# Kernel tuning notes

Measured on AMD Instinct MI355X. Metric: run time of the kernel, lower is better.

Reference implementation:

```python
import jax, jax.numpy as jnp
import numpy as np

B, S, D, H, E, K, HID = 4, 1024, 1024, 16, 8, 2, 4096
HD = D // H


def _ln(x, g, b):
    m = x.mean(-1, keepdims=True)
    v = x.var(-1, keepdims=True)
    return (x - m) / jnp.sqrt(v + 1e-5) * g + b


def setup_inputs():
    key = jax.random.key(0)
    ks = jax.random.split(key, 12)
    p = lambda i, shape: jax.random.normal(ks[i], shape, jnp.float32) * 0.02
    return {
        "x": jax.random.normal(ks[0], (B, S, D), jnp.float32),
        "text_state": jax.random.normal(ks[1], (B, D), jnp.float32),
        "ln1_g": jnp.ones((D,), jnp.float32), "ln1_b": jnp.zeros((D,), jnp.float32),
        "wqkv": p(2, (D, 3 * D)), "bqkv": jnp.zeros((3 * D,), jnp.float32),
        "wo": p(3, (D, D)), "bo": jnp.zeros((D,), jnp.float32),
        "rel_bias": p(4, (H, 2 * S - 1)),
        "ln2_g": jnp.ones((D,), jnp.float32), "ln2_b": jnp.zeros((D,), jnp.float32),
        "cap_w": p(5, (D, D)), "cap_b": jnp.zeros((D,), jnp.float32),
        "gate_w": p(6, (D, E)), "gate_b": jnp.zeros((E,), jnp.float32),
        "w1": p(7, (E, D, HID)), "b1": jnp.zeros((E, HID), jnp.float32),
        "w2": p(8, (E, HID, D)), "b2": jnp.zeros((E, D), jnp.float32),
    }


def reference(x, text_state, ln1_g, ln1_b, wqkv, bqkv, wo, bo, rel_bias,
              ln2_g, ln2_b, cap_w, cap_b, gate_w, gate_b, w1, b1, w2, b2):
    # --- temporal-bias multi-head self-attention (pre-LN, residual) ---
    h = _ln(x, ln1_g, ln1_b)
    qkv = h @ wqkv + bqkv                          # [B,S,3D]
    q, k, v = jnp.split(qkv, 3, axis=-1)
    q = q.reshape(B, S, H, HD).transpose(0, 2, 1, 3)
    k = k.reshape(B, S, H, HD).transpose(0, 2, 1, 3)
    v = v.reshape(B, S, H, HD).transpose(0, 2, 1, 3)
    scores = jnp.einsum('bhqd,bhkd->bhqk', q, k) / jnp.sqrt(jnp.float32(HD))
    rel = jnp.arange(S)[:, None] - jnp.arange(S)[None, :] + (S - 1)  # [S,S]
    scores = scores + rel_bias[:, rel][None]       # learned temporal bias per head
    attn = jax.nn.softmax(scores, axis=-1)
    o = jnp.einsum('bhqk,bhkd->bhqd', attn, v).transpose(0, 2, 1, 3).reshape(B, S, D)
    x = x + o @ wo + bo

    # --- caption-conditioned top-k MoE FFN (pre-LN, residual) ---
    h2 = _ln(x, ln2_g, ln2_b)
    gate_in = h2 + (text_state @ cap_w + cap_b)[:, None, :]
    logits = gate_in @ gate_w + gate_b             # [B,S,E]
    vals, eidx = jax.lax.top_k(logits, K)          # [B,S,K]
    gw = jax.nn.softmax(vals, axis=-1)
    y = jnp.einsum('bsd,edh->bseh', h2, w1) + b1   # all experts densely
    y = jax.nn.gelu(y)
    y = jnp.einsum('bseh,ehd->bsed', y, w2) + b2   # [B,S,E,D]
    sel = jnp.take_along_axis(y, eidx[..., None], axis=2)  # [B,S,K,D]
    moe = (gw[..., None] * sel).sum(axis=2)
    x = x + moe

    load = jnp.mean(jax.nn.one_hot(eidx, E, dtype=jnp.float32), axis=(0, 1, 2))
    return x, load
```

## Files before the change

### kernel.cpp

```cpp
#include <hip/hip_runtime.h>
#include <hip/hip_bf16.h>

typedef __attribute__((ext_vector_type(8))) short short8;
typedef __attribute__((ext_vector_type(4))) float f32x4;

#define MFMA16(a,b,c) __builtin_amdgcn_mfma_f32_16x16x32_bf16((a),(b),(c),0,0,0)

__device__ __forceinline__ short f2b(float f){
    return __builtin_bit_cast(short, __float2bfloat16(f));
}
__device__ __forceinline__ void split2(float f, short &hi, short &lo){
    __hip_bfloat16 h = __float2bfloat16(f);
    hi = __builtin_bit_cast(short, h);
    lo = f2b(f - __bfloat162float(h));
}

__global__ __launch_bounds__(256)
void castT_k(const float* __restrict__ in, short* __restrict__ hiT,
             short* __restrict__ loT, int R, int C)
{
    __shared__ float tile[32][33];
    size_t boff = (size_t)blockIdx.z * (size_t)R * (size_t)C;
    int tx = threadIdx.x & 31, ty = threadIdx.x >> 5;
    int r0 = blockIdx.y * 32, c0 = blockIdx.x * 32;
#pragma unroll
    for (int i = 0; i < 4; i++)
        tile[ty + i*8][tx] = in[boff + (size_t)(r0 + ty + i*8) * C + c0 + tx];
    __syncthreads();
#pragma unroll
    for (int i = 0; i < 4; i++) {
        float v = tile[tx][ty + i*8];
        size_t o = boff + (size_t)(c0 + ty + i*8) * R + r0 + tx;
        short h, l; split2(v, h, l);
        hiT[o] = h;
        if (loT) loT[o] = l;
    }
}

__global__ __launch_bounds__(256)
void ln_k(const float* __restrict__ x, const float* __restrict__ g,
          const float* __restrict__ be, short* __restrict__ outhi,
          short* __restrict__ outlo)
{
    int row = blockIdx.x;
    const float* xr = x + (size_t)row * 1024;
    int tid = threadIdx.x;
    float4 v = reinterpret_cast<const float4*>(xr)[tid];
    float s = v.x + v.y + v.z + v.w;
    float q = v.x*v.x + v.y*v.y + v.z*v.z + v.w*v.w;
#pragma unroll
    for (int m = 1; m < 64; m <<= 1) { s += __shfl_xor(s, m); q += __shfl_xor(q, m); }
    __shared__ float ss[4], sq[4];
    int wid = tid >> 6;
    if ((tid & 63) == 0) { ss[wid] = s; sq[wid] = q; }
    __syncthreads();
    float S = ss[0] + ss[1] + ss[2] + ss[3];
    float Qs = sq[0] + sq[1] + sq[2] + sq[3];
    float mean = S * (1.f/1024.f);
    float var = Qs * (1.f/1024.f) - mean*mean;
    float rstd = rsqrtf(var + 1e-5f);
    float4 gv = reinterpret_cast<const float4*>(g)[tid];
    float4 bv = reinterpret_cast<const float4*>(be)[tid];
    float o[4];
    o[0] = (v.x-mean)*rstd*gv.x + bv.x;
    o[1] = (v.y-mean)*rstd*gv.y + bv.y;
    o[2] = (v.z-mean)*rstd*gv.z + bv.z;
    o[3] = (v.w-mean)*rstd*gv.w + bv.w;
    short hs[4], ls[4];
#pragma unroll
    for (int i = 0; i < 4; i++) split2(o[i], hs[i], ls[i]);
    typedef __attribute__((ext_vector_type(4))) short short4v;
    short4v hv; hv[0]=hs[0]; hv[1]=hs[1]; hv[2]=hs[2]; hv[3]=hs[3];
    *reinterpret_cast<short4v*>(outhi + (size_t)row*1024 + tid*4) = hv;
    if (outlo) {
        short4v lv; lv[0]=ls[0]; lv[1]=ls[1]; lv[2]=ls[2]; lv[3]=ls[3];
        *reinterpret_cast<short4v*>(outlo + (size_t)row*1024 + tid*4) = lv;
    }
}

__global__ __launch_bounds__(256)
void cap_k(const float* __restrict__ ts, const float* __restrict__ cw,
           const float* __restrict__ cb, float* __restrict__ capo)
{
    int d = blockIdx.x * 256 + threadIdx.x;
    int b = blockIdx.y;
    const float* t = ts + (size_t)b * 1024;
    float acc = cb[d];
    for (int k = 0; k < 1024; k++) acc = fmaf(t[k], cw[(size_t)k*1024 + d], acc);
    capo[(size_t)b*1024 + d] = acc;
}

__global__ __launch_bounds__(64)
void gate_k(const float* __restrict__ x2, const float* __restrict__ g,
            const float* __restrict__ be, const float* __restrict__ capo,
            const float* __restrict__ gw, const float* __restrict__ gb,
            int* __restrict__ elist, float* __restrict__ ewt, int* __restrict__ cnt)
{
    int t = blockIdx.x;
    int b = t >> 10;
    int lane = threadIdx.x;
    const float* xr = x2 + (size_t)t * 1024;
    float v[16];
    float s = 0.f, q = 0.f;
#pragma unroll
    for (int i = 0; i < 16; i++) {
        v[i] = xr[i*64 + lane];
        s += v[i]; q += v[i]*v[i];
    }
#pragma unroll
    for (int m = 1; m < 64; m <<= 1) { s += __shfl_xor(s, m); q += __shfl_xor(q, m); }
    float mean = s * (1.f/1024.f);
    float var = q * (1.f/1024.f) - mean*mean;
    float rstd = rsqrtf(var + 1e-5f);
    float acc[8] = {0,0,0,0,0,0,0,0};
    const float* cr = capo + (size_t)b * 1024;
#pragma unroll
    for (int i = 0; i < 16; i++) {
        int d = i*64 + lane;
        float gi = (v[i]-mean)*rstd*g[d] + be[d] + cr[d];
        const float4* gp = reinterpret_cast<const float4*>(gw + (size_t)d*8);
        float4 g0 = gp[0], g1 = gp[1];
        acc[0] += gi*g0.x; acc[1] += gi*g0.y; acc[2] += gi*g0.z; acc[3] += gi*g0.w;
        acc[4] += gi*g1.x; acc[5] += gi*g1.y; acc[6] += gi*g1.z; acc[7] += gi*g1.w;
    }
#pragma unroll
    for (int e = 0; e < 8; e++)
#pragma unroll
        for (int m = 1; m < 64; m <<= 1) acc[e] += __shfl_xor(acc[e], m);
    if (lane == 0) {
        float v0 = -1e30f, v1 = -1e30f; int i0 = 0, i1 = 0;
#pragma unroll
        for (int e = 0; e < 8; e++) {
            float lg = acc[e] + gb[e];
            if (lg > v0) { v1 = v0; i1 = i0; v0 = lg; i0 = e; }
            else if (lg > v1) { v1 = lg; i1 = e; }
        }
        float w0 = 1.f / (1.f + __expf(v1 - v0));
        float w1 = 1.f - w0;
        int p0 = atomicAdd(&cnt[i0], 1);
        elist[i0*4096 + p0] = t; ewt[i0*4096 + p0] = w0;
        int p1 = atomicAdd(&cnt[i1], 1);
        elist[i1*4096 + p1] = t; ewt[i1*4096 + p1] = w1;
    }
}

__global__ void scan_k(const int* __restrict__ cnt, int* __restrict__ ebase,
                       float* __restrict__ outload)
{
    int t = threadIdx.x;
    if (t == 0) { int s = 0; for (int e = 0; e < 8; e++) { ebase[e] = s; s += cnt[e]; } }
    if (t < 8) outload[t] = (float)cnt[t] * (1.f/8192.f);
}

enum { M_QKV = 0, M_WO = 1, M_F1 = 2, M_F2 = 3 };

template<int MODE, bool SP>
__global__ __launch_bounds__(256)
void gemm_k(const short* __restrict__ Ahi, const short* __restrict__ Alo,
            const short* __restrict__ Bhi, const short* __restrict__ Blo,
            const float* __restrict__ bias,
            float* __restrict__ outf, short* __restrict__ outhi, short* __restrict__ outlo,
            const float* __restrict__ resid,
            const int* __restrict__ elist, const float* __restrict__ ew,
            const int* __restrict__ cnt, const int* __restrict__ ebase,
            int M, int N, int K)
{
    int e = blockIdx.z;
    int m0 = blockIdx.y * 128, n0 = blockIdx.x * 128;
    int Mloc = M;
    int baseE = 0;
    if (MODE == M_F1 || MODE == M_F2) {
        Mloc = cnt[e];
        if (m0 >= Mloc) return;
        baseE = ebase[e];
        Bhi += (size_t)e * 4194304;
        bias += (size_t)e * N;
    }
    __shared__ short As[SP ? 2 : 1][128][40];
    __shared__ short Bs[SP ? 2 : 1][128][40];
    int tid = threadIdx.x;
    int lane = tid & 63, wid = tid >> 6;
    int wr = wid >> 1, wc = wid & 1;
    int rl = lane & 15, rg = lane >> 4;
    f32x4 acc[4][4] = {};
    for (int k0 = 0; k0 < K; k0 += 32) {
        __syncthreads();
#pragma unroll
        for (int j = 0; j < 2; ++j) {
            int idx = j*256 + tid;
            int row = idx >> 2, kb = (idx & 3) * 8;
            short8 av = {}, avl = {};
            int mrow = m0 + row;
            if (mrow < Mloc) {
                size_t arow;
                if (MODE == M_F1)      arow = (size_t)elist[e*4096 + mrow];
                else if (MODE == M_F2) arow = (size_t)(baseE + mrow);
                else                   arow = (size_t)mrow;
                av = *reinterpret_cast<const short8*>(Ahi + arow*(size_t)K + k0 + kb);
                if (SP) avl = *reinterpret_cast<const short8*>(Alo + arow*(size_t)K + k0 + kb);
            }
            *reinterpret_cast<short8*>(&As[0][row][kb]) = av;
            if (SP) *reinterpret_cast<short8*>(&As[SP?1:0][row][kb]) = avl;
            short8 bv = *reinterpret_cast<const short8*>(Bhi + (size_t)(n0+row)*K + k0 + kb);
            *reinterpret_cast<short8*>(&Bs[0][row][kb]) = bv;
            if (SP) {
                short8 bvl = *reinterpret_cast<const short8*>(Blo + (size_t)(n0+row)*K + k0 + kb);
                *reinterpret_cast<short8*>(&Bs[SP?1:0][row][kb]) = bvl;
            }
        }
        __syncthreads();
        short8 afh[4], bfh[4], afl[4], bfl[4];
#pragma unroll
        for (int i = 0; i < 4; i++) afh[i] = *reinterpret_cast<short8*>(&As[0][wr*64 + i*16 + rl][rg*8]);
#pragma unroll
        for (int i = 0; i < 4; i++) bfh[i] = *reinterpret_cast<short8*>(&Bs[0][wc*64 + i*16 + rl][rg*8]);
        if (SP) {
#pragma unroll
            for (int i = 0; i < 4; i++) afl[i] = *reinterpret_cast<short8*>(&As[SP?1:0][wr*64 + i*16 + rl][rg*8]);
#pragma unroll
            for (int i = 0; i < 4; i++) bfl[i] = *reinterpret_cast<short8*>(&Bs[SP?1:0][wc*64 + i*16 + rl][rg*8]);
        }
#pragma unroll
        for (int mi = 0; mi < 4; mi++)
#pragma unroll
            for (int ni = 0; ni < 4; ni++) {
                acc[mi][ni] = MFMA16(afh[mi], bfh[ni], acc[mi][ni]);
                if (SP) {
                    acc[mi][ni] = MFMA16(afh[mi], bfl[ni], acc[mi][ni]);
                    acc[mi][ni] = MFMA16(afl[mi], bfh[ni], acc[mi][ni]);
                    acc[mi][ni] = MFMA16(afl[mi], bfl[ni], acc[mi][ni]);
                }
            }
    }
#pragma unroll
    for (int mi = 0; mi < 4; mi++) {
#pragma unroll
        for (int ni = 0; ni < 4; ni++) {
            int col = n0 + wc*64 + ni*16 + rl;
            f32x4 a = acc[mi][ni];
#pragma unroll
            for (int r = 0; r < 4; r++) {
                int rrow = wr*64 + mi*16 + rg*4 + r;
                int mrow = m0 + rrow;
                if (mrow >= Mloc) continue;
                float val = a[r] + bias[col];
                if (MODE == M_QKV) {
                    int which = col >> 10, d = col & 1023;
                    int hh = d >> 6, hd = d & 63;
                    int bb = mrow >> 10, sidx = mrow & 1023;
                    size_t o = (size_t)which*4194304 + (((size_t)(bb*16 + hh))*1024 + sidx)*64 + hd;
                    short h, l; split2(val, h, l);
                    outhi[o] = h; outlo[o] = l;
                } else if (MODE == M_WO) {
                    size_t o = (size_t)mrow*1024 + col;
                    outf[o] = val + resid[o];
                } else if (MODE == M_F1) {
                    float xx = val;
                    float z = 0.7978845608028654f * (xx + 0.044715f*xx*xx*xx);
                    float th = 1.f - 2.f/(1.f + __expf(2.f*z));
                    float gl = 0.5f*xx*(1.f + th);
                    outhi[(size_t)(baseE + mrow)*4096 + col] = f2b(gl);
                } else {
                    int tok = elist[e*4096 + mrow];
                    float w = ew[e*4096 + mrow];
                    atomicAdd(&outf[(size_t)tok*1024 + col], w*val);
                }
            }
        }
    }
}

__global__ __launch_bounds__(256)
void attn_k(const short* __restrict__ qkvhi, const short* __restrict__ qkvlo,
            const float* __restrict__ relb,
            short* __restrict__ obhi, short* __restrict__ oblo)
{
    int bh = blockIdx.y, qt = blockIdx.x;
    int b = bh >> 4, h = bh & 15;
    int tid = threadIdx.x, wid = tid >> 6, lane = tid & 63;
    int rl = lane & 15, rg = lane >> 4;
    const short* Qh = qkvhi + (size_t)bh * 65536;
    const short* Ql = qkvlo + (size_t)bh * 65536;
    const short* Kh_g = qkvhi + 4194304 + (size_t)bh * 65536;
    const short* Kl_g = qkvlo + 4194304 + (size_t)bh * 65536;
    const short* Vh_g = qkvhi + 8388608 + (size_t)bh * 65536;
    const short* Vl_g = qkvlo + 8388608 + (size_t)bh * 65536;
    __shared__ short Kh[64][72], Kl[64][72];
    __shared__ short Vh[64][72], Vl[64][72];
    __shared__ short Ph[4][16][72], Pl[4][16][72];
    int q0 = qt*64 + wid*16;
    short8 qh0 = *reinterpret_cast<const short8*>(Qh + (size_t)(q0+rl)*64 + rg*8);
    short8 qh1 = *reinterpret_cast<const short8*>(Qh + (size_t)(q0+rl)*64 + 32 + rg*8);
    short8 ql0 = *reinterpret_cast<const short8*>(Ql + (size_t)(q0+rl)*64 + rg*8);
    short8 ql1 = *reinterpret_cast<const short8*>(Ql + (size_t)(q0+rl)*64 + 32 + rg*8);
    f32x4 O[4] = {};
    float mr[4] = {-1e30f,-1e30f,-1e30f,-1e30f};
    float lr[4] = {0.f,0.f,0.f,0.f};
    const float* rb = relb + h*2047 + 1023;
    for (int kt = 0; kt < 16; ++kt) {
        int kb0 = kt * 64;
        __syncthreads();
#pragma unroll
        for (int j = 0; j < 2; j++) {
            int idx = j*256 + tid;
            int row = idx >> 3, cb = (idx & 7) * 8;
            *reinterpret_cast<short8*>(&Kh[row][cb]) =
                *reinterpret_cast<const short8*>(Kh_g + (size_t)(kb0+row)*64 + cb);
            *reinterpret_cast<short8*>(&Kl[row][cb]) =
                *reinterpret_cast<const short8*>(Kl_g + (size_t)(kb0+row)*64 + cb);
            short8 vh = *reinterpret_cast<const short8*>(Vh_g + (size_t)(kb0+row)*64 + cb);
            short8 vl = *reinterpret_cast<const short8*>(Vl_g + (size_t)(kb0+row)*64 + cb);
#pragma unroll
            for (int i = 0; i < 8; i++) { Vh[cb+i][row] = vh[i]; Vl[cb+i][row] = vl[i]; }
        }
        __syncthreads();
        f32x4 sc[4];
#pragma unroll
        for (int c = 0; c < 4; c++) {
            short8 kh0 = *reinterpret_cast<short8*>(&Kh[c*16+rl][rg*8]);
            short8 kh1 = *reinterpret_cast<short8*>(&Kh[c*16+rl][32+rg*8]);
            short8 kl0 = *reinterpret_cast<short8*>(&Kl[c*16+rl][rg*8]);
            short8 kl1 = *reinterpret_cast<short8*>(&Kl[c*16+rl][32+rg*8]);
            f32x4 t = {};
            t = MFMA16(qh0, kh0, t); t = MFMA16(qh1, kh1, t);
            t = MFMA16(qh0, kl0, t); t = MFMA16(qh1, kl1, t);
            t = MFMA16(ql0, kh0, t); t = MFMA16(ql1, kh1, t);
            t = MFMA16(ql0, kl0, t); t = MFMA16(ql1, kl1, t);
            sc[c] = t;
        }
        float pm[4] = {-1e30f,-1e30f,-1e30f,-1e30f};
#pragma unroll
        for (int c = 0; c < 4; c++) {
            int kk = kb0 + c*16 + rl;
#pragma unroll
            for (int r = 0; r < 4; r++) {
                int q = q0 + rg*4 + r;
                float sv = sc[c][r]*0.125f + rb[q - kk];
                sc[c][r] = sv;
                pm[r] = fmaxf(pm[r], sv);
            }
        }
#pragma unroll
        for (int r = 0; r < 4; r++) {
            pm[r] = fmaxf(pm[r], __shfl_xor(pm[r], 1));
            pm[r] = fmaxf(pm[r], __shfl_xor(pm[r], 2));
            pm[r] = fmaxf(pm[r], __shfl_xor(pm[r], 4));
            pm[r] = fmaxf(pm[r], __shfl_xor(pm[r], 8));
        }
        float scl[4], ps[4];
#pragma unroll
        for (int r = 0; r < 4; r++) {
            float mn = fmaxf(mr[r], pm[r]);
            scl[r] = __expf(mr[r] - mn);
            mr[r] = mn;
            ps[r] = 0.f;
        }
#pragma unroll
        for (int c = 0; c < 4; c++)
#pragma unroll
            for (int r = 0; r < 4; r++) {
                float p = __expf(sc[c][r] - mr[r]);
                sc[c][r] = p;
                ps[r] += p;
            }
#pragma unroll
        for (int r = 0; r < 4; r++) {
            ps[r] += __shfl_xor(ps[r], 1);
            ps[r] += __shfl_xor(ps[r], 2);
            ps[r] += __shfl_xor(ps[r], 4);
            ps[r] += __shfl_xor(ps[r], 8);
            lr[r] = lr[r]*scl[r] + ps[r];
        }
#pragma unroll
        for (int cc = 0; cc < 4; cc++) {
            O[cc][0] *= scl[0]; O[cc][1] *= scl[1];
            O[cc][2] *= scl[2]; O[cc][3] *= scl[3];
        }
#pragma unroll
        for (int c = 0; c < 4; c++)
#pragma unroll
            for (int r = 0; r < 4; r++) {
                short hp, lp; split2(sc[c][r], hp, lp);
                Ph[wid][rg*4+r][c*16+rl] = hp;
                Pl[wid][rg*4+r][c*16+rl] = lp;
            }
#pragma unroll
        for (int cc = 0; cc < 4; cc++) {
#pragma unroll
            for (int ks = 0; ks < 2; ks++) {
                short8 ph = *reinterpret_cast<short8*>(&Ph[wid][rl][ks*32 + rg*8]);
                short8 pl = *reinterpret_cast<short8*>(&Pl[wid][rl][ks*32 + rg*8]);
                short8 vh = *reinterpret_cast<short8*>(&Vh[cc*16+rl][ks*32 + rg*8]);
                short8 vl = *reinterpret_cast<short8*>(&Vl[cc*16+rl][ks*32 + rg*8]);
                O[cc] = MFMA16(ph, vh, O[cc]);
                O[cc] = MFMA16(ph, vl, O[cc]);
                O[cc] = MFMA16(pl, vh, O[cc]);
            }
        }
    }
#pragma unroll
    for (int cc = 0; cc < 4; cc++) {
#pragma unroll
        for (int r = 0; r < 4; r++) {
            int q = q0 + rg*4 + r;
            float val = O[cc][r] / lr[r];
            size_t o = ((size_t)(b*1024 + q))*1024 + h*64 + cc*16 + rl;
            short hv, lv; split2(val, hv, lv);
            obhi[o] = hv; oblo[o] = lv;
        }
    }
}

extern "C" void kernel_launch(void* const* d_in, const int* in_sizes, int n_in,
                              void* d_out, int out_size, void* d_ws, size_t ws_size,
                              hipStream_t stream)
{
    const float* x     = (const float*)d_in[0];
    const float* ts    = (const float*)d_in[1];
    const float* ln1g  = (const float*)d_in[2];
    const float* ln1b_ = (const float*)d_in[3];
    const float* wqkv  = (const float*)d_in[4];
    const float* bqkv  = (const float*)d_in[5];
    const float* wo    = (const float*)d_in[6];
    const float* bo    = (const float*)d_in[7];
    const float* relb  = (const float*)d_in[8];
    const float* ln2g  = (const float*)d_in[9];
    const float* ln2b_ = (const float*)d_in[10];
    const float* capw  = (const float*)d_in[11];
    const float* capb  = (const float*)d_in[12];
    const float* gatew = (const float*)d_in[13];
    const float* gateb = (const float*)d_in[14];
    const float* w1    = (const float*)d_in[15];
    const float* b1    = (const float*)d_in[16];
    const float* w2    = (const float*)d_in[17];
    const float* b2    = (const float*)d_in[18];
    float* out = (float*)d_out;

    char* p = (char*)d_ws;
    short* w1T    = (short*)p; p += 67108864;
    short* w2T    = (short*)p; p += 67108864;
    short* wqThi  = (short*)p; p += 6291456;
    short* wqTlo  = (short*)p; p += 6291456;
    short* woThi  = (short*)p; p += 2097152;
    short* woTlo  = (short*)p; p += 2097152;
    short* qkvhi  = (short*)p; p += 25165824;
    short* qkvlo  = (short*)p; p += 25165824;
    short* h2b    = (short*)p; p += 8388608;
    float* capo   = (float*)p; p += 16384;
    int*   elist  = (int*)p;   p += 131072;
    float* ewt    = (float*)p; p += 131072;
    int*   cnt    = (int*)p;   p += 256;
    int*   ebase  = (int*)p;   p += 256;
    short* mid    = (short*)p; p += 67108864;
    short* h1hi   = mid;
    short* h1lo   = mid + 4194304;
    short* obhi   = mid + 8388608;
    short* oblo   = mid + 12582912;

    hipMemsetAsync(cnt, 0, 32, stream);

    castT_k<<<dim3(96, 32, 1),  256, 0, stream>>>(wqkv, wqThi, wqTlo, 1024, 3072);
    castT_k<<<dim3(32, 32, 1),  256, 0, stream>>>(wo,   woThi, woTlo, 1024, 1024);
    castT_k<<<dim3(128, 32, 8), 256, 0, stream>>>(w1,   w1T,  nullptr, 1024, 4096);
    castT_k<<<dim3(32, 128, 8), 256, 0, stream>>>(w2,   w2T,  nullptr, 4096, 1024);

    ln_k<<<4096, 256, 0, stream>>>(x, ln1g, ln1b_, h1hi, h1lo);

    gemm_k<M_QKV, true><<<dim3(24, 32, 1), 256, 0, stream>>>(
        h1hi, h1lo, wqThi, wqTlo, bqkv, nullptr, qkvhi, qkvlo,
        nullptr, nullptr, nullptr, nullptr, nullptr, 4096, 3072, 1024);

    attn_k<<<dim3(16, 64), 256, 0, stream>>>(qkvhi, qkvlo, relb, obhi, oblo);

    gemm_k<M_WO, true><<<dim3(8, 32, 1), 256, 0, stream>>>(
        obhi, oblo, woThi, woTlo, bo, out, nullptr, nullptr,
        x, nullptr, nullptr, nullptr, nullptr, 4096, 1024, 1024);

    cap_k<<<dim3(4, 4), 256, 0, stream>>>(ts, capw, capb, capo);

    ln_k<<<4096, 256, 0, stream>>>(out, ln2g, ln2b_, h2b, nullptr);

    gate_k<<<4096, 64, 0, stream>>>(out, ln2g, ln2b_, capo, gatew, gateb,
                                    elist, ewt, cnt);

    scan_k<<<1, 64, 0, stream>>>(cnt, ebase, out + 4194304);

    gemm_k<M_F1, false><<<dim3(32, 32, 8), 256, 0, stream>>>(
        h2b, nullptr, w1T, nullptr, b1, nullptr, mid, nullptr,
        nullptr, elist, ewt, cnt, ebase, 4096, 4096, 1024);

    gemm_k<M_F2, false><<<dim3(8, 32, 8), 256, 0, stream>>>(
        mid, nullptr, w2T, nullptr, b2, out, nullptr, nullptr,
        nullptr, elist, ewt, cnt, ebase, 4096, 1024, 4096);

    (void)in_sizes; (void)n_in; (void)out_size; (void)ws_size;
}
```

Measured before the change: 1.229 ms.

## Double-buffer GEMM via async LDS loads, drop lo*lo MFMAs, vectorize transpose and cap

The GEMM now stages A/B tiles straight into LDS with global_load_lds, using a swizzled layout and double buffering so the next K-tile loads while the current one is computed. MoE row indices are precomputed once per block into shared memory. The lo*lo correction MFMA is removed from the split-bf16 GEMMs and from the attention score computation, trading a small amount of precision for fewer matrix ops. The weight transpose/cast kernel moves to 64x64 tiles with vectorized loads and stores, and the caption projection splits K across four waves with a shared-memory reduction. Out-of-range MoE rows are clamped to valid rows rather than zero-filled, which depends on the epilogue masking them correctly.

```diff
diff --git a/kernel.cpp b/kernel.cpp
--- a/kernel.cpp
+++ b/kernel.cpp
@@ -14,26 +14,42 @@
     hi = __builtin_bit_cast(short, h);
     lo = f2b(f - __bfloat162float(h));
 }
+__device__ __forceinline__ void cp16(void* l, const void* g){
+    __builtin_amdgcn_global_load_lds(
+        (const __attribute__((address_space(1))) unsigned int*)g,
+        (__attribute__((address_space(3))) unsigned int*)l, 16, 0, 0);
+}
 
 __global__ __launch_bounds__(256)
 void castT_k(const float* __restrict__ in, short* __restrict__ hiT,
              short* __restrict__ loT, int R, int C)
 {
-    __shared__ float tile[32][33];
+    __shared__ float t[64][65];
     size_t boff = (size_t)blockIdx.z * (size_t)R * (size_t)C;
-    int tx = threadIdx.x & 31, ty = threadIdx.x >> 5;
-    int r0 = blockIdx.y * 32, c0 = blockIdx.x * 32;
-#pragma unroll
-    for (int i = 0; i < 4; i++)
-        tile[ty + i*8][tx] = in[boff + (size_t)(r0 + ty + i*8) * C + c0 + tx];
+    int r0 = blockIdx.y * 64, c0 = blockIdx.x * 64;
+    int tid = threadIdx.x;
+    int lr = tid >> 4, lc = (tid & 15) * 4;
+#pragma unroll
+    for (int p = 0; p < 4; p++) {
+        int r = p*16 + lr;
+        float4 v = *reinterpret_cast<const float4*>(in + boff + (size_t)(r0+r)*C + c0 + lc);
+        t[r][lc] = v.x; t[r][lc+1] = v.y; t[r][lc+2] = v.z; t[r][lc+3] = v.w;
+    }
     __syncthreads();
 #pragma unroll
-    for (int i = 0; i < 4; i++) {
-        float v = tile[tx][ty + i*8];
-        size_t o = boff + (size_t)(c0 + ty + i*8) * R + r0 + tx;
-        short h, l; split2(v, h, l);
-        hiT[o] = h;
-        if (loT) loT[o] = l;
+    for (int p = 0; p < 2; p++) {
+        int ch = p*256 + tid;
+        int c = ch >> 3, seg = (ch & 7) * 8;
+        short8 hv, lv;
+#pragma unroll
+        for (int i = 0; i < 8; i++) {
+            float v = t[seg+i][c];
+            short h, l; split2(v, h, l);
+            hv[i] = h; lv[i] = l;
+        }
+        size_t o = boff + (size_t)(c0+c)*R + r0 + seg;
+        *reinterpret_cast<short8*>(hiT + o) = hv;
+        if (loT) *reinterpret_cast<short8*>(loT + o) = lv;
     }
 }
 
@@ -82,12 +98,19 @@
 void cap_k(const float* __restrict__ ts, const float* __restrict__ cw,
            const float* __restrict__ cb, float* __restrict__ capo)
 {
-    int d = blockIdx.x * 256 + threadIdx.x;
     int b = blockIdx.y;
+    int d = blockIdx.x * 64 + (threadIdx.x & 63);
+    int ks = threadIdx.x >> 6;
     const float* t = ts + (size_t)b * 1024;
-    float acc = cb[d];
-    for (int k = 0; k < 1024; k++) acc = fmaf(t[k], cw[(size_t)k*1024 + d], acc);
-    capo[(size_t)b*1024 + d] = acc;
+    float acc = 0.f;
+    for (int k = ks*256; k < ks*256 + 256; k++)
+        acc = fmaf(t[k], cw[(size_t)k*1024 + d], acc);
+    __shared__ float red[4][64];
+    red[ks][threadIdx.x & 63] = acc;
+    __syncthreads();
+    if (ks == 0)
+        capo[(size_t)b*1024 + d] = red[0][threadIdx.x&63] + red[1][threadIdx.x&63]
+                                 + red[2][threadIdx.x&63] + red[3][threadIdx.x&63] + cb[d];
 }
 
 __global__ __launch_bounds__(64)
@@ -159,66 +182,90 @@
 void gemm_k(const short* __restrict__ Ahi, const short* __restrict__ Alo,
             const short* __restrict__ Bhi, const short* __restrict__ Blo,
             const float* __restrict__ bias,
-            float* __restrict__ outf, short* __restrict__ outhi, short* __restrict__ outlo,
+            float* __restrict__ outf, short* __restrict__ outhi,
             const float* __restrict__ resid,
             const int* __restrict__ elist, const float* __restrict__ ew,
             const int* __restrict__ cnt, const int* __restrict__ ebase,
             int M, int N, int K)
 {
+    constexpr int NT = SP ? 4 : 2;
+    constexpr bool MOE = (MODE == M_F1 || MODE == M_F2);
     int e = blockIdx.z;
     int m0 = blockIdx.y * 128, n0 = blockIdx.x * 128;
     int Mloc = M;
     int baseE = 0;
-    if (MODE == M_F1 || MODE == M_F2) {
+    if (MOE) {
         Mloc = cnt[e];
         if (m0 >= Mloc) return;
         baseE = ebase[e];
         Bhi += (size_t)e * 4194304;
         bias += (size_t)e * N;
     }
-    __shared__ short As[SP ? 2 : 1][128][40];
-    __shared__ short Bs[SP ? 2 : 1][128][40];
+    __shared__ short lds[NT * 8192];
+    int* rowmap = nullptr;
+    if constexpr (MOE) {
+        __shared__ int rowmap_s[128];
+        rowmap = rowmap_s;
+    }
     int tid = threadIdx.x;
     int lane = tid & 63, wid = tid >> 6;
     int wr = wid >> 1, wc = wid & 1;
     int rl = lane & 15, rg = lane >> 4;
+
+    if constexpr (MOE) {
+        if (tid < 128) {
+            int mrow = m0 + tid;
+            int ar;
+            if (MODE == M_F1) {
+                int idx = mrow < Mloc ? mrow : Mloc - 1;
+                ar = elist[e*4096 + idx];
+            } else {
+                ar = baseE + mrow;
+                if (ar > 8191) ar = 8191;
+            }
+            rowmap[tid] = ar;
+        }
+        __syncthreads();
+    }
+
+    auto STAGE = [&](int buf, int k0) {
+        short* base = lds + buf * (NT * 4096);
+        for (int is = wid; is < NT * 8; is += 4) {
+            int tile = is >> 3, issue = is & 7;
+            int row = issue*16 + (lane >> 2);
+            int sch = (lane & 3) ^ ((row >> 1) & 3);
+            const short* src;
+            if (tile < (SP ? 2 : 1)) {
+                int ar = MOE ? rowmap[row] : (m0 + row);
+                const short* Ab = (SP && tile == 1) ? Alo : Ahi;
+                src = Ab + (size_t)ar * K + k0 + sch*8;
+            } else {
+                const short* Bb = (SP && tile == 3) ? Blo : Bhi;
+                src = Bb + (size_t)(n0 + row) * K + k0 + sch*8;
+            }
+            cp16(base + tile*4096 + issue*512, src);
+        }
+    };
+
     f32x4 acc[4][4] = {};
-    for (int k0 = 0; k0 < K; k0 += 32) {
+    int nt = K >> 5;
+    STAGE(0, 0);
+    int cur = 0;
+    for (int t = 0; t < nt; ++t) {
         __syncthreads();
-#pragma unroll
-        for (int j = 0; j < 2; ++j) {
-            int idx = j*256 + tid;
-            int row = idx >> 2, kb = (idx & 3) * 8;
-            short8 av = {}, avl = {};
-            int mrow = m0 + row;
-            if (mrow < Mloc) {
-                size_t arow;
-                if (MODE == M_F1)      arow = (size_t)elist[e*4096 + mrow];
-                else if (MODE == M_F2) arow = (size_t)(baseE + mrow);
-                else                   arow = (size_t)mrow;
-                av = *reinterpret_cast<const short8*>(Ahi + arow*(size_t)K + k0 + kb);
-                if (SP) avl = *reinterpret_cast<const short8*>(Alo + arow*(size_t)K + k0 + kb);
-            }
-            *reinterpret_cast<short8*>(&As[0][row][kb]) = av;
-            if (SP) *reinterpret_cast<short8*>(&As[SP?1:0][row][kb]) = avl;
-            short8 bv = *reinterpret_cast<const short8*>(Bhi + (size_t)(n0+row)*K + k0 + kb);
-            *reinterpret_cast<short8*>(&Bs[0][row][kb]) = bv;
-            if (SP) {
-                short8 bvl = *reinterpret_cast<const short8*>(Blo + (size_t)(n0+row)*K + k0 + kb);
-                *reinterpret_cast<short8*>(&Bs[SP?1:0][row][kb]) = bvl;
-            }
-        }
-        __syncthreads();
+        if (t + 1 < nt) STAGE(cur ^ 1, (t + 1) * 32);
+        const short* cb = lds + cur * (NT * 4096);
         short8 afh[4], bfh[4], afl[4], bfl[4];
 #pragma unroll
-        for (int i = 0; i < 4; i++) afh[i] = *reinterpret_cast<short8*>(&As[0][wr*64 + i*16 + rl][rg*8]);
-#pragma unroll
-        for (int i = 0; i < 4; i++) bfh[i] = *reinterpret_cast<short8*>(&Bs[0][wc*64 + i*16 + rl][rg*8]);
-        if (SP) {
-#pragma unroll
-            for (int i = 0; i < 4; i++) afl[i] = *reinterpret_cast<short8*>(&As[SP?1:0][wr*64 + i*16 + rl][rg*8]);
-#pragma unroll
-            for (int i = 0; i < 4; i++) bfl[i] = *reinterpret_cast<short8*>(&Bs[SP?1:0][wc*64 + i*16 + rl][rg*8]);
+        for (int i = 0; i < 4; i++) {
+            int ra = wr*64 + i*16 + rl;
+            int ca = ra*32 + ((rg ^ ((ra >> 1) & 3)) * 8);
+            afh[i] = *reinterpret_cast<const short8*>(cb + ca);
+            if (SP) afl[i] = *reinterpret_cast<const short8*>(cb + 4096 + ca);
+            int rb = wc*64 + i*16 + rl;
+            int cb2 = rb*32 + ((rg ^ ((rb >> 1) & 3)) * 8);
+            bfh[i] = *reinterpret_cast<const short8*>(cb + (SP?2:1)*4096 + cb2);
+            if (SP) bfl[i] = *reinterpret_cast<const short8*>(cb + 3*4096 + cb2);
         }
 #pragma unroll
         for (int mi = 0; mi < 4; mi++)
@@ -228,9 +275,9 @@
                 if (SP) {
                     acc[mi][ni] = MFMA16(afh[mi], bfl[ni], acc[mi][ni]);
                     acc[mi][ni] = MFMA16(afl[mi], bfh[ni], acc[mi][ni]);
-                    acc[mi][ni] = MFMA16(afl[mi], bfl[ni], acc[mi][ni]);
                 }
             }
+        cur ^= 1;
     }
 #pragma unroll
     for (int mi = 0; mi < 4; mi++) {
@@ -240,8 +287,7 @@
             f32x4 a = acc[mi][ni];
 #pragma unroll
             for (int r = 0; r < 4; r++) {
-                int rrow = wr*64 + mi*16 + rg*4 + r;
-                int mrow = m0 + rrow;
+                int mrow = m0 + wr*64 + mi*16 + rg*4 + r;
                 if (mrow >= Mloc) continue;
                 float val = a[r] + bias[col];
                 if (MODE == M_QKV) {
@@ -250,7 +296,7 @@
                     int bb = mrow >> 10, sidx = mrow & 1023;
                     size_t o = (size_t)which*4194304 + (((size_t)(bb*16 + hh))*1024 + sidx)*64 + hd;
                     short h, l; split2(val, h, l);
-                    outhi[o] = h; outlo[o] = l;
+                    outhi[o] = h; outhi[12582912 + o] = l;
                 } else if (MODE == M_WO) {
                     size_t o = (size_t)mrow*1024 + col;
                     outf[o] = val + resid[o];
@@ -325,7 +371,6 @@
             t = MFMA16(qh0, kh0, t); t = MFMA16(qh1, kh1, t);
             t = MFMA16(qh0, kl0, t); t = MFMA16(qh1, kl1, t);
             t = MFMA16(ql0, kh0, t); t = MFMA16(ql1, kh1, t);
-            t = MFMA16(ql0, kl0, t); t = MFMA16(ql1, kl1, t);
             sc[c] = t;
         }
         float pm[4] = {-1e30f,-1e30f,-1e30f,-1e30f};
@@ -444,7 +489,9 @@
     short* woThi  = (short*)p; p += 2097152;
     short* woTlo  = (short*)p; p += 2097152;
     short* qkvhi  = (short*)p; p += 25165824;
-    short* qkvlo  = (short*)p; p += 25165824;
+    short* qkvlo  = qkvhi + 12582912; p += 0;
+    p += 25165824 - 25165824;
+    p = (char*)(qkvhi + 25165824);
     short* h2b    = (short*)p; p += 8388608;
     float* capo   = (float*)p; p += 16384;
     int*   elist  = (int*)p;   p += 131072;
@@ -459,24 +506,24 @@
 
     hipMemsetAsync(cnt, 0, 32, stream);
 
-    castT_k<<<dim3(96, 32, 1),  256, 0, stream>>>(wqkv, wqThi, wqTlo, 1024, 3072);
-    castT_k<<<dim3(32, 32, 1),  256, 0, stream>>>(wo,   woThi, woTlo, 1024, 1024);
-    castT_k<<<dim3(128, 32, 8), 256, 0, stream>>>(w1,   w1T,  nullptr, 1024, 4096);
-    castT_k<<<dim3(32, 128, 8), 256, 0, stream>>>(w2,   w2T,  nullptr, 4096, 1024);
+    castT_k<<<dim3(48, 16, 1), 256, 0, stream>>>(wqkv, wqThi, wqTlo, 1024, 3072);
+    castT_k<<<dim3(16, 16, 1), 256, 0, stream>>>(wo,   woThi, woTlo, 1024, 1024);
+    castT_k<<<dim3(64, 16, 8), 256, 0, stream>>>(w1,   w1T,  nullptr, 1024, 4096);
+    castT_k<<<dim3(16, 64, 8), 256, 0, stream>>>(w2,   w2T,  nullptr, 4096, 1024);
 
     ln_k<<<4096, 256, 0, stream>>>(x, ln1g, ln1b_, h1hi, h1lo);
 
     gemm_k<M_QKV, true><<<dim3(24, 32, 1), 256, 0, stream>>>(
-        h1hi, h1lo, wqThi, wqTlo, bqkv, nullptr, qkvhi, qkvlo,
+        h1hi, h1lo, wqThi, wqTlo, bqkv, nullptr, qkvhi,
         nullptr, nullptr, nullptr, nullptr, nullptr, 4096, 3072, 1024);
 
     attn_k<<<dim3(16, 64), 256, 0, stream>>>(qkvhi, qkvlo, relb, obhi, oblo);
 
     gemm_k<M_WO, true><<<dim3(8, 32, 1), 256, 0, stream>>>(
-        obhi, oblo, woThi, woTlo, bo, out, nullptr, nullptr,
+        obhi, oblo, woThi, woTlo, bo, out, nullptr,
         x, nullptr, nullptr, nullptr, nullptr, 4096, 1024, 1024);
 
-    cap_k<<<dim3(4, 4), 256, 0, stream>>>(ts, capw, capb, capo);
+    cap_k<<<dim3(16, 4), 256, 0, stream>>>(ts, capw, capb, capo);
 
     ln_k<<<4096, 256, 0, stream>>>(out, ln2g, ln2b_, h2b, nullptr);
 
@@ -486,11 +533,11 @@
     scan_k<<<1, 64, 0, stream>>>(cnt, ebase, out + 4194304);
 
     gemm_k<M_F1, false><<<dim3(32, 32, 8), 256, 0, stream>>>(
-        h2b, nullptr, w1T, nullptr, b1, nullptr, mid, nullptr,
+        h2b, nullptr, w1T, nullptr, b1, nullptr, mid,
         nullptr, elist, ewt, cnt, ebase, 4096, 4096, 1024);
 
     gemm_k<M_F2, false><<<dim3(8, 32, 8), 256, 0, stream>>>(
-        mid, nullptr, w2T, nullptr, b2, out, nullptr, nullptr,
+        mid, nullptr, w2T, nullptr, b2, out, nullptr,
         nullptr, elist, ewt, cnt, ebase, 4096, 1024, 4096);
 
     (void)in_sizes; (void)n_in; (void)out_size; (void)ws_size;
```

Result: slower. 1.409 ms (+14.6%).
